# Performance work log

Hardware: AMD Instinct MI355X
Metric: run time of the kernel (lower is better)

## Reference

```python
import jax, jax.numpy as jnp
import numpy as np

# ---- static hyperparameters (mirror init_kwargs) ----
L_MAX = 3
N_MAX_L = [8, 6, 4, 2]            # radial basis size per l (precomputer.n_max_l)
N_CHANNELS = 32                   # num_element_channels
K_MAX_L = [n * N_CHANNELS for n in N_MAX_L]   # [256, 192, 128, 64]
SH_SIZES = [2 * l + 1 for l in range(L_MAX + 1)]  # [1,3,5,7]
MP_SCALING = 0.1
NU_SCALING = 0.1
NU_MAX = 2                        # max_correlation_order_per_layer
N_LAYERS = 2                      # num_message_passing_layers

# Fixed CG coupling tensors for all valid (l1, l2, L) with |l1-l2|<=L<=min(l1+l2, L_MAX).
# (Deterministic stand-ins for real Clebsch-Gordan coefficients; same sparsity/coupling
# structure and identical in fwd and fwdbwd modules.)
_rng = np.random.RandomState(0)
CG = {}
for _l1 in range(L_MAX + 1):
    for _l2 in range(L_MAX + 1):
        for _L in range(abs(_l1 - _l2), min(_l1 + _l2, L_MAX) + 1):
            CG[(_l1, _l2, _L)] = jnp.asarray(
                (_rng.randn(2 * _l1 + 1, 2 * _l2 + 1, 2 * _L + 1) * 0.2).astype(np.float32))


def split_l(x, sizes):
    out, i = [], 0
    for s in sizes:
        out.append(x[:, i:i + s])
        i += s
    return out


def embed_centers(feats, emb):
    # feats[l]: [N, 2l+1, n_l*C]; multiply channel block c by per-atom embedding emb[:, c]
    C = emb.shape[1]
    out = []
    for f in feats:
        n, m, k = f.shape
        out.append((f.reshape(n, m, k // C, C) * emb[:, None, None, :]).reshape(n, m, k))
    return out


def tensor_product(A, B):
    # per-atom CG tensor product, channel-aligned with truncation to min k
    n = A[0].shape[0]
    out = [jnp.zeros((n, 2 * L + 1, K_MAX_L[L]), A[0].dtype) for L in range(L_MAX + 1)]
    for (l1, l2, L), cg in CG.items():
        kk = min(K_MAX_L[l1], K_MAX_L[l2], K_MAX_L[L])
        t = jnp.einsum('nak,nbk,abM->nMk', A[l1][:, :, :kk], B[l2][:, :, :kk], cg)
        out[L] = out[L].at[:, :, :kk].add(t)
    return out


def cg_iterate(feats):
    # CGIterator: nu_max-1 iterated tensor products with residual accumulation
    g = feats
    for _ in range(NU_MAX - 1):
        tp = tensor_product(g, feats)
        g = [g[l] + NU_SCALING * tp[l] for l in range(L_MAX + 1)]
    return g


def invariant_mp(rb_l, sh_l, centers, emb_nbr, n_atoms):
    # spherical expansion: scatter rb x sh x neighbor-embedding over pairs -> centers
    out = []
    for l in range(L_MAX + 1):
        # [P, 2l+1, n_l, C] -> [P, 2l+1, k_l]
        msg = sh_l[l][:, :, None, None] * rb_l[l][:, None, :, None] * emb_nbr[:, None, None, :]
        msg = msg.reshape(msg.shape[0], 2 * l + 1, -1)
        out.append(MP_SCALING * jax.ops.segment_sum(msg, centers, num_segments=n_atoms))
    return out


def equivariant_mp(rb_l, sh_l, centers, neighbors, feats, n_atoms):
    # pair messages: CG-couple radially weighted SH edge features with neighbor features
    edge = [sh_l[l] * rb_l[l].sum(-1, keepdims=True) for l in range(L_MAX + 1)]  # [P, 2l+1]
    out = [jnp.zeros((n_atoms, 2 * L + 1, K_MAX_L[L]), feats[0].dtype) for L in range(L_MAX + 1)]
    for (l1, l2, L), cg in CG.items():
        kk = min(K_MAX_L[l2], K_MAX_L[L])
        w = jnp.einsum('pa,abM->pbM', edge[l1], cg)        # [P, 2l2+1, 2L+1]
        fg = feats[l2][neighbors, :, :kk]                   # gather: [P, 2l2+1, kk]
        msg = jnp.einsum('pbM,pbk->pMk', w, fg)             # [P, 2L+1, kk]
        out[L] = out[L].at[:, :, :kk].add(
            MP_SCALING * jax.ops.segment_sum(msg, centers, num_segments=n_atoms))
    return out


def setup_inputs() -> dict:
    key = jax.random.key(0)
    ks = jax.random.split(key, 8)
    N, P = 5000, 100000
    return {
        'sh': jax.random.normal(ks[0], (P, sum(SH_SIZES)), dtype=jnp.float32),
        'rb': jax.random.uniform(ks[1], (P, sum(N_MAX_L)), dtype=jnp.float32),
        'emb_table': jax.random.normal(ks[2], (4, N_CHANNELS), dtype=jnp.float32),
        'w_energy': jax.random.normal(ks[3], (K_MAX_L[0], 1), dtype=jnp.float32) * 0.05,
        'b_energy': jax.random.normal(ks[4], (1,), dtype=jnp.float32),
        'species_idx': jax.random.randint(ks[5], (N,), 0, 4, dtype=jnp.int32),
        'centers': jax.random.randint(ks[6], (P,), 0, N, dtype=jnp.int32),
        'neighbors': jax.random.randint(ks[7], (P,), 0, N, dtype=jnp.int32),
    }


def reference(sh, rb, emb_table, w_energy, b_energy, species_idx, centers, neighbors):
    n_atoms = species_idx.shape[0]
    sh_l = split_l(sh * NU_SCALING, SH_SIZES)   # nu_scaling applied to spherical harmonics
    rb_l = split_l(rb, N_MAX_L)
    center_emb = emb_table[species_idx]          # [N, C]
    emb_nbr = center_emb[neighbors]              # [P, C]
    # invariant message passing -> spherical expansion, then first CG iteration
    feats = invariant_mp(rb_l, sh_l, centers, emb_nbr, n_atoms)
    feats = cg_iterate(feats)
    # remaining equivariant message-passing layers
    for _ in range(N_LAYERS - 1):
        ef = embed_centers(feats, center_emb)
        mp = equivariant_mp(rb_l, sh_l, centers, neighbors, ef, n_atoms)
        feats = cg_iterate(mp)
    feats = embed_centers(feats, center_emb)
    energies = feats[0] @ w_energy + b_energy    # [N, 1, 1]
    return energies
```

## Files before the change

kernel.cpp:

```cpp
#include <hip/hip_runtime.h>
#include <vector>
#include <cmath>
#include <cstdint>

constexpr int KLc[4]  = {256,192,128,64};
constexpr int NMLc[4] = {8,6,4,2};
constexpr int SHBc[5] = {0,1,4,9,16};
constexpr int RBBc[5] = {0,8,14,18,20};
constexpr int FBc[5]  = {0,256,832,1472,1920};
constexpr int NCMB = 34, CGTOT = 3436, FTOT = 1920;

struct Combos { int l1[NCMB], l2[NCMB], L[NCMB], cgoff[NCMB], kk[NCMB]; };
constexpr Combos make_combos(){
  Combos c{}; int n=0, cg=0;
  for(int a=0;a<=3;a++)for(int b=0;b<=3;b++){
    int lo=a>b?a-b:b-a, hi=(a+b<3)?(a+b):3;
    for(int L=lo;L<=hi;L++){
      c.l1[n]=a; c.l2[n]=b; c.L[n]=L; c.cgoff[n]=cg;
      int mx=a>b?a:b; if(L>mx) mx=L; c.kk[n]=KLc[mx];
      cg+=(2*a+1)*(2*b+1)*(2*L+1); n++;
    }
  }
  return c;
}
constexpr Combos CB = make_combos();
static_assert(CB.cgoff[NCMB-1] + 7*7*7 == CGTOT, "cg size");

struct Grp { int cnt[4]; int list[4][12]; };
constexpr Grp make_Lg(){ Grp g{}; for(int i=0;i<NCMB;i++){ int L=CB.L[i]; g.list[L][g.cnt[L]++]=i; } return g; }
constexpr Grp LG = make_Lg();

struct Rows { int sh[64], rb[64], off[64]; };
constexpr Rows make_rows(){ Rows r{}; int i=0;
  for(int l=0;l<4;l++)for(int m=0;m<2*l+1;m++)for(int n=0;n<NMLc[l];n++){
    r.sh[i]=SHBc[l]+m; r.rb[i]=RBBc[l]+n; r.off[i]=FBc[l]+m*KLc[l]+n*32; i++; }
  for(;i<64;i++){ r.sh[i]=0; r.rb[i]=0; r.off[i]=0; }
  return r; }
constexpr Rows RWS = make_rows();

constexpr int NSL=425, NG=16, MAXS=32, MAXR=4, RPAD=149;
constexpr int JB=48, DEPTH=6;
static_assert(JB % DEPTH == 0, "slot rotation alignment");
constexpr int NTILE=30;

constexpr int iabs_(int x){ return x<0?-x:x; }
__host__ __device__ constexpr bool sl_valid(int l1,int l2,int kt){ return l2<=3-kt && iabs_(l1-l2)<=3-kt; }

__host__ __device__ constexpr int rb_base(int kt,int l1,int l2){
  int base=0;
  for(int p=0;p<4;p++)for(int q=0;q<4;q++){
    if(p==l1 && q==l2) return base;
    if(sl_valid(p,q,kt)) base += (2*p+1)*(2*q+1);
  }
  return base;
}

struct EqTab {
  int ns[NG];
  unsigned char eidx[NG][MAXS];
  unsigned char fidx[NG][MAXS];
  short         srow[NG][MAXS];
  unsigned char sph [NG][MAXS];
  int nr[NG];
  short roff[NG][MAXR];
  int total;
};
constexpr EqTab make_eqtab(){
  EqTab T{};
  int tl2[NTILE]{}, tkt[NTILE]{}, tbb[NTILE]{}, tsz[NTILE]{}; int nt=0;
  for(int l2=0;l2<4;l2++)for(int kt=0;kt<4-l2;kt++)for(int b=0;b<2*l2+1;b++){
    int sz=0;
    for(int l1=0;l1<4;l1++) if(sl_valid(l1,l2,kt)) sz+=2*l1+1;
    tl2[nt]=l2; tkt[nt]=kt; tbb[nt]=b; tsz[nt]=sz; nt++;
  }
  int tg[NTILE]{}; bool used[NTILE]{}; int gload[NG]{};
  for(int it=0; it<nt; it++){
    int best=-1;
    for(int i=0;i<nt;i++) if(!used[i] && (best<0 || tsz[i]>tsz[best])) best=i;
    used[best]=true;
    int g=0; for(int j=1;j<NG;j++) if(gload[j]<gload[g]) g=j;
    tg[best]=g; gload[g]+=tsz[best];
  }
  int total=0;
  for(int g=0; g<NG; g++){
    for(int ti=0; ti<nt; ti++){
      if(tg[ti]!=g) continue;
      const int l2=tl2[ti], kt=tkt[ti], b=tbb[ti];
      const int rowoff = FBc[l2] + b*KLc[l2] + kt*64;
      const int ri = T.nr[g]; T.roff[g][T.nr[g]++] = (short)rowoff;
      for(int l1=0;l1<4;l1++){
        if(!sl_valid(l1,l2,kt)) continue;
        for(int a=0;a<2*l1+1;a++){
          int s = T.ns[g]++;
          T.eidx[g][s] = (unsigned char)(SHBc[l1]+a);
          int rbi = rb_base(kt,l1,l2) + a*(2*l2+1) + b;
          int ph, sr;
          if(kt==0){ if(l1<=2){ ph=0; sr=rbi; } else { ph=1; sr=rbi-144; } }
          else { ph=kt+1; sr=rbi; }
          T.sph[g][s]=(unsigned char)ph; T.srow[g][s]=(short)sr;
          T.fidx[g][s]=(unsigned char)ri;
          total++;
        }
      }
    }
    for(int i=1;i<T.ns[g];i++){
      unsigned char e=T.eidx[g][i], f=T.fidx[g][i], p=T.sph[g][i]; short r=T.srow[g][i];
      int k=i-1;
      while(k>=0 && T.eidx[g][k]>e){
        T.eidx[g][k+1]=T.eidx[g][k]; T.fidx[g][k+1]=T.fidx[g][k];
        T.sph[g][k+1]=T.sph[g][k];   T.srow[g][k+1]=T.srow[g][k]; k--;
      }
      T.eidx[g][k+1]=e; T.fidx[g][k+1]=f; T.sph[g][k+1]=p; T.srow[g][k+1]=r;
    }
  }
  T.total=total;
  return T;
}
constexpr EqTab ET = make_eqtab();
static_assert(ET.total==NSL, "slice count");
constexpr bool chk_ns(){ for(int g=0;g<NG;g++) if(ET.ns[g]>MAXS) return false; return true; }
constexpr bool chk_nr(){ for(int g=0;g<NG;g++) if(ET.nr[g]>MAXR) return false; return true; }
constexpr int sum_nr(){ int s=0; for(int g=0;g<NG;g++) s+=ET.nr[g]; return s; }
static_assert(chk_ns(), "MAXS");
static_assert(chk_nr(), "MAXR");
static_assert(sum_nr()==NTILE, "no row duplication across groups");

struct CAsg { int cnt[NG]; unsigned char ci[NG][8]; };
constexpr CAsg make_casg(){
  CAsg C{}; bool used[NCMB]{}; int load[NG]{};
  for(int it=0; it<NCMB; it++){
    int best=-1, bc=-1;
    for(int i=0;i<NCMB;i++) if(!used[i]){
      int c=(2*CB.l1[i]+1)*(2*CB.l2[i]+1)*(2*CB.L[i]+1);
      if(c>bc){bc=c;best=i;}
    }
    used[best]=true;
    int g=0; for(int j=1;j<NG;j++) if(load[j]<load[g]) g=j;
    C.ci[g][C.cnt[g]++]=(unsigned char)best; load[g]+=bc;
  }
  return C;
}
constexpr CAsg CA = make_casg();
constexpr bool chk_ca(){ for(int g=0;g<NG;g++) if(CA.cnt[g]>8) return false; return true; }
static_assert(chk_ca(), "CA cap");

__host__ __device__ constexpr bool combo_in_phase(int ci,int ph){
  int l1=CB.l1[ci], l2=CB.l2[ci], L=CB.L[ci];
  if(ph==0) return l1<=2;
  if(ph==1) return l1==3;
  int kt=ph-1;
  return (l2<=3-kt) && (L<=3-kt);
}
__host__ __device__ constexpr int phase_kt(int ph){ return ph<=1?0:ph-1; }
__host__ __device__ constexpr int phase_rbadj(int ph){ return ph==1?144:0; }

namespace nprng {
struct MT {
  uint32_t mt[624]; int mti; bool has_g; double g;
  void seed(uint32_t s){ for(int i=0;i<624;i++){ mt[i]=s; s=1812433253u*(s^(s>>30))+(uint32_t)i+1u; } mti=624; has_g=false; g=0.0; }
  uint32_t u32(){
    if(mti>=624){
      for(int i=0;i<624;i++){
        uint32_t y=(mt[i]&0x80000000u)|(mt[(i+1)%624]&0x7fffffffu);
        mt[i]=mt[(i+397)%624]^(y>>1)^((y&1u)?0x9908b0dfu:0u);
      }
      mti=0;
    }
    uint32_t y=mt[mti++];
    y^=y>>11; y^=(y<<7)&0x9d2c5680u; y^=(y<<15)&0xefc60000u; y^=y>>18;
    return y;
  }
  double dbl(){ uint32_t a=u32()>>5, b=u32()>>6; return (a*67108864.0+b)/9007199254740992.0; }
  double gauss(){
    if(has_g){ has_g=false; return g; }
    double f,x1,x2,r2;
    do{ x1=2.0*dbl()-1.0; x2=2.0*dbl()-1.0; r2=x1*x1+x2*x2; }while(r2>=1.0||r2==0.0);
    f=sqrt(-2.0*log(r2)/r2);
    g=f*x1; has_g=true; return f*x2;
  }
};
}
static std::vector<float> build_cg(){
  nprng::MT r; r.seed(0);
  std::vector<float> v; v.reserve(CGTOT);
  for(int l1=0;l1<=3;l1++)for(int l2=0;l2<=3;l2++){
    int lo = l1>l2? l1-l2 : l2-l1;
    int hi = (l1+l2<3)? (l1+l2) : 3;
    for(int L=lo;L<=hi;L++){
      int n=(2*l1+1)*(2*l2+1)*(2*L+1);
      for(int i=0;i<n;i++) v.push_back((float)(r.gauss()*0.2));
    }
  }
  return v;
}

__global__ __launch_bounds__(256) void k_cemb(const float* __restrict__ emb_table,
    const int* __restrict__ species, float* __restrict__ cemb, int* __restrict__ counts, int N){
  int i = blockIdx.x*256 + threadIdx.x;
  if(i < N) counts[i] = 0;
  if(i < N*32){ int n = i>>5, c = i&31; cemb[i] = emb_table[species[n]*32 + c]; }
}

__global__ __launch_bounds__(256) void k_hist(const int* __restrict__ centers, int* counts, int P){
  int i = blockIdx.x*256 + threadIdx.x;
  if(i < P) atomicAdd(&counts[centers[i]], 1);
}

__global__ __launch_bounds__(256) void k_scan(const int* __restrict__ counts,
    int* __restrict__ offsets, int* __restrict__ cursor, int N){
  __shared__ int part[256];
  const int t = threadIdx.x;
  const int CH = (N + 255)/256;
  const int lo = t*CH;
  int hi = (t+1)*CH; if(hi > N) hi = N;
  int s = 0;
  for(int i=lo;i<hi;i++) s += counts[i];
  part[t] = s; __syncthreads();
  const int own = s;
  for(int d=1; d<256; d<<=1){
    int v = (t>=d)? part[t-d] : 0;
    __syncthreads();
    part[t] += v;
    __syncthreads();
  }
  int run = part[t] - own;
  for(int i=lo;i<hi;i++){ offsets[i]=run; cursor[i]=run; run += counts[i]; }
  if(t==255) offsets[N] = part[255];
}

__global__ __launch_bounds__(256) void k_scatter(const int* __restrict__ centers,
    int* cursor, int* __restrict__ perm, int P){
  int i = blockIdx.x*256 + threadIdx.x;
  if(i < P){ int c = centers[i]; int pos = atomicAdd(&cursor[c], 1); perm[pos] = i; }
}

__global__ __launch_bounds__(256) void k_permute(const float* __restrict__ sh,
    const float* __restrict__ rb, const int* __restrict__ nbrs, const int* __restrict__ perm,
    float* __restrict__ edge_p, int* __restrict__ nbrp, int P){
  int u = blockIdx.x*256 + threadIdx.x;
  int pos = u>>4, i = u&15;
  if(pos >= P) return;
  int p = perm[pos];
  if(i==0) nbrp[pos] = nbrs[p];
  int l = (i==0)?0:(i<4)?1:(i<9)?2:3;
  float s=0.f;
  for(int n=RBBc[l]; n<RBBc[l+1]; n++) s += rb[p*20+n];
  edge_p[(size_t)pos*16+i] = sh[p*16+i]*0.1f*s;
}

__global__ __launch_bounds__(256) void k_inv(const float* __restrict__ sh, const float* __restrict__ rb,
    const float* __restrict__ cemb, const int* __restrict__ nbrs, const int* __restrict__ offsets,
    const int* __restrict__ perm, float* __restrict__ feats){
  const int a = blockIdx.x, t = threadIdx.x;
  __shared__ float sh_s[8][16], rb_s[8][20], emb_s[8][32], shrb_s[8][60];
  const int c = t & 31, rg = t >> 5;
  float acc[8];
  #pragma unroll
  for(int j=0;j<8;j++) acc[j] = 0.f;
  const int beg = offsets[a], cnt = offsets[a+1]-beg;
  for(int jb=0; jb<cnt; jb+=8){
    __syncthreads();
    for(int u=t; u<8*36; u+=256){
      int j=u/36, i=u-36*j;
      if(jb+j<cnt){
        int p=perm[beg+jb+j];
        if(i<16) sh_s[j][i]=sh[p*16+i]*0.1f;
        else     rb_s[j][i-16]=rb[p*20+i-16];
      }
    }
    for(int u=t; u<8*32; u+=256){
      int j=u>>5, i=u&31;
      if(jb+j<cnt){ int nb=nbrs[perm[beg+jb+j]]; emb_s[j][i]=cemb[(size_t)nb*32+i]; }
    }
    __syncthreads();
    for(int u=t; u<8*60; u+=256){
      int j=u/60, r=u-60*j;
      if(jb+j<cnt) shrb_s[j][r] = sh_s[j][RWS.sh[r]] * rb_s[j][RWS.rb[r]];
    }
    __syncthreads();
    const int jm = (cnt-jb<8)?(cnt-jb):8;
    for(int j=0;j<jm;j++){
      const float e = emb_s[j][c];
      #pragma unroll
      for(int q=0;q<8;q++){ int r=rg+8*q; if(r<60) acc[q]=fmaf(shrb_s[j][r], e, acc[q]); }
    }
  }
  #pragma unroll
  for(int q=0;q<8;q++){
    int r = rg + 8*q;
    if(r < 60) feats[(size_t)a*FTOT + RWS.off[r] + c] = 0.1f * acc[q];
  }
}

__device__ __forceinline__ float cg_u(const float* __restrict__ cg, int idx){
  return cg[__builtin_amdgcn_readfirstlane(idx)];
}
__global__ __launch_bounds__(256) void k_tp(float* __restrict__ feats, const float* __restrict__ cg){
  const int a = blockIdx.x, t = threadIdx.x;
  __shared__ float f_s[FTOT];
  float* fa = feats + (size_t)a*FTOT;
  for(int i=t;i<FTOT;i+=256)  f_s[i]  = fa[i];
  __syncthreads();
  #pragma unroll
  for(int L=0; L<4; L++){
    const int KLL = KLc[L], nL = 2*L+1;
    const int nel = nL*KLL;
    for(int e=t; e<nel; e+=256){
      const int M = e / KLL, k = e - M*KLL;
      float acc = 0.f;
      #pragma unroll
      for(int gi=0; gi<LG.cnt[L]; gi++){
        const int ci = LG.list[L][gi];
        const int l1 = CB.l1[ci], l2 = CB.l2[ci];
        if(k < CB.kk[ci]){
          const int n2 = 2*l2+1;
          #pragma unroll
          for(int aa=0; aa<2*l1+1; aa++){
            const float Av = f_s[FBc[l1] + aa*KLc[l1] + k];
            #pragma unroll
            for(int b=0; b<n2; b++)
              acc += cg_u(cg, CB.cgoff[ci] + (aa*n2+b)*nL + M) * (Av * f_s[FBc[l2] + b*KLc[l2] + k]);
          }
        }
      }
      fa[FBc[L] + M*KLL + k] = f_s[FBc[L] + M*KLL + k] + 0.1f*acc;
    }
  }
}

template<int G,int PH,int U>
__device__ __forceinline__ void contract_combos(const float* __restrict__ stageT,
    float* __restrict__ out_s, const float* __restrict__ cg, int lane){
  if constexpr (U < CA.cnt[G]) {
    constexpr int ci = CA.ci[G][U];
    if constexpr (combo_in_phase(ci,PH)) {
      constexpr int l1=CB.l1[ci], l2=CB.l2[ci], L=CB.L[ci];
      constexpr int n1=2*l1+1, n2=2*l2+1, nL=2*L+1;
      constexpr int kt=phase_kt(PH);
      constexpr int rbase = rb_base(kt,l1,l2) - phase_rbadj(PH);
      float oa[nL];
      #pragma unroll
      for(int M=0;M<nL;M++) oa[M]=0.f;
      #pragma unroll
      for(int aa=0;aa<n1;aa++){
        #pragma unroll
        for(int b=0;b<n2;b++){
          const float sv = stageT[lane*RPAD + rbase + aa*n2 + b];
          #pragma unroll
          for(int M=0;M<nL;M++)
            oa[M] = fmaf(cg[CB.cgoff[ci] + (aa*n2+b)*nL + M], sv, oa[M]);
        }
      }
      #pragma unroll
      for(int M=0;M<nL;M++)
        atomicAdd(&out_s[FBc[L] + M*KLc[L] + kt*64 + lane], oa[M]);
    }
    contract_combos<G,PH,U+1>(stageT,out_s,cg,lane);
  }
}

template<int G,int PH>
__device__ __forceinline__ void eq_phase(const float* acc, float* stageT, float* out_s,
    const float* __restrict__ cg, int lane){
  __syncthreads();
  #pragma unroll
  for(int s=0;s<ET.ns[G];s++){
    if(ET.sph[G][s]==PH) stageT[lane*RPAD + ET.srow[G][s]] = acc[s];
  }
  __syncthreads();
  contract_combos<G,PH,0>(stageT,out_s,cg,lane);
}

template<int G>
__device__ __forceinline__ void eq_load_pair(float* fg, float& ce, int nb, int lane,
    const float* __restrict__ featsA, const float* __restrict__ cemb){
  ce = cemb[(size_t)nb*32 + (lane&31)];
  const float* fp = featsA + (size_t)nb*FTOT + lane;
  #pragma unroll
  for(int r=0;r<ET.nr[G];r++) fg[r] = fp[ET.roff[G][r]];
}

template<int G>
__device__ __forceinline__ void eq_compute_pair(float* acc, const float* fg, float ce,
    const float* edge_row){
  constexpr int NR = ET.nr[G];
  float fgc[NR];
  #pragma unroll
  for(int r=0;r<NR;r++) fgc[r] = fg[r]*ce;
  float edv = 0.f;
  #pragma unroll
  for(int s=0;s<ET.ns[G];s++){
    if(s==0 || ET.eidx[G][s]!=ET.eidx[G][s-1])
      edv = edge_row[ET.eidx[G][s]];
    acc[s] = fmaf(edv, fgc[ET.fidx[G][s]], acc[s]);
  }
}

template<int G>
__device__ __forceinline__ void eq_group_main(
    const int a, const int t, const int lane,
    const float* __restrict__ edge_p, const int* __restrict__ nbrp,
    const float* __restrict__ cemb, const int* __restrict__ offsets,
    const float* __restrict__ featsA, float* __restrict__ featsB,
    const float* __restrict__ cg,
    float* stageT, float* out_s, float* edge_s, int* nb_s){
  constexpr int NS = ET.ns[G], NR = ET.nr[G];
  float acc[NS];
  #pragma unroll
  for(int s=0;s<NS;s++) acc[s]=0.f;
  for(int i=t;i<FTOT;i+=1024) out_s[i]=0.f;
  const int beg = offsets[a], cnt = offsets[a+1]-beg;
  float fgS[DEPTH][NR]; float ceS[DEPTH];
  #pragma unroll
  for(int s=0;s<DEPTH;s++){
    int nb = (s<cnt)? nbrp[beg+s] : 0;
    eq_load_pair<G>(fgS[s], ceS[s], nb, lane, featsA, cemb);
  }
  for(int jb=0; jb<cnt; jb+=JB){
    __syncthreads();
    if(t < JB*16){
      int j = t>>4;
      if(jb+j < cnt) edge_s[t] = edge_p[(size_t)(beg+jb)*16 + t];
    }
    if(t < JB) nb_s[t] = (jb+t < cnt) ? nbrp[beg+jb+t] : 0;
    __syncthreads();
    const int jm = (cnt-jb<JB)?(cnt-jb):JB;
    for(int j=0;j<jm;j+=DEPTH){
      #pragma unroll
      for(int s=0;s<DEPTH;s++){
        if(j+s < jm){
          eq_compute_pair<G>(acc, fgS[s], ceS[s], edge_s + (j+s)*16);
          int q = jb+j+s+DEPTH;
          int nb = (q<cnt) ? ((q-jb<JB)? nb_s[q-jb] : nbrp[beg+q]) : 0;
          eq_load_pair<G>(fgS[s], ceS[s], nb, lane, featsA, cemb);
        }
      }
    }
  }
  eq_phase<G,0>(acc,stageT,out_s,cg,lane);
  eq_phase<G,1>(acc,stageT,out_s,cg,lane);
  eq_phase<G,2>(acc,stageT,out_s,cg,lane);
  eq_phase<G,3>(acc,stageT,out_s,cg,lane);
  eq_phase<G,4>(acc,stageT,out_s,cg,lane);
  __syncthreads();
  float* ob = featsB + (size_t)a*FTOT;
  for(int i=t;i<FTOT;i+=1024) ob[i] = 0.1f*out_s[i];
}

__global__ __launch_bounds__(1024,4) void k_eq2(const float* __restrict__ edge_p,
    const int* __restrict__ nbrp, const float* __restrict__ cemb,
    const int* __restrict__ offsets, const float* __restrict__ featsA,
    float* __restrict__ featsB, const float* __restrict__ cg){
  __shared__ float stageT[64*RPAD];
  __shared__ float out_s[FTOT];
  __shared__ float edge_s[JB*16];
  __shared__ int   nb_s[JB];
  const int a = blockIdx.x, t = threadIdx.x, lane = t&63, g = t>>6;
  switch(g){
    case 0:  eq_group_main<0 >(a,t,lane,edge_p,nbrp,cemb,offsets,featsA,featsB,cg,stageT,out_s,edge_s,nb_s); break;
    case 1:  eq_group_main<1 >(a,t,lane,edge_p,nbrp,cemb,offsets,featsA,featsB,cg,stageT,out_s,edge_s,nb_s); break;
    case 2:  eq_group_main<2 >(a,t,lane,edge_p,nbrp,cemb,offsets,featsA,featsB,cg,stageT,out_s,edge_s,nb_s); break;
    case 3:  eq_group_main<3 >(a,t,lane,edge_p,nbrp,cemb,offsets,featsA,featsB,cg,stageT,out_s,edge_s,nb_s); break;
    case 4:  eq_group_main<4 >(a,t,lane,edge_p,nbrp,cemb,offsets,featsA,featsB,cg,stageT,out_s,edge_s,nb_s); break;
    case 5:  eq_group_main<5 >(a,t,lane,edge_p,nbrp,cemb,offsets,featsA,featsB,cg,stageT,out_s,edge_s,nb_s); break;
    case 6:  eq_group_main<6 >(a,t,lane,edge_p,nbrp,cemb,offsets,featsA,featsB,cg,stageT,out_s,edge_s,nb_s); break;
    case 7:  eq_group_main<7 >(a,t,lane,edge_p,nbrp,cemb,offsets,featsA,featsB,cg,stageT,out_s,edge_s,nb_s); break;
    case 8:  eq_group_main<8 >(a,t,lane,edge_p,nbrp,cemb,offsets,featsA,featsB,cg,stageT,out_s,edge_s,nb_s); break;
    case 9:  eq_group_main<9 >(a,t,lane,edge_p,nbrp,cemb,offsets,featsA,featsB,cg,stageT,out_s,edge_s,nb_s); break;
    case 10: eq_group_main<10>(a,t,lane,edge_p,nbrp,cemb,offsets,featsA,featsB,cg,stageT,out_s,edge_s,nb_s); break;
    case 11: eq_group_main<11>(a,t,lane,edge_p,nbrp,cemb,offsets,featsA,featsB,cg,stageT,out_s,edge_s,nb_s); break;
    case 12: eq_group_main<12>(a,t,lane,edge_p,nbrp,cemb,offsets,featsA,featsB,cg,stageT,out_s,edge_s,nb_s); break;
    case 13: eq_group_main<13>(a,t,lane,edge_p,nbrp,cemb,offsets,featsA,featsB,cg,stageT,out_s,edge_s,nb_s); break;
    case 14: eq_group_main<14>(a,t,lane,edge_p,nbrp,cemb,offsets,featsA,featsB,cg,stageT,out_s,edge_s,nb_s); break;
    default: eq_group_main<15>(a,t,lane,edge_p,nbrp,cemb,offsets,featsA,featsB,cg,stageT,out_s,edge_s,nb_s); break;
  }
}

__global__ __launch_bounds__(256) void k_energy(const float* __restrict__ feats,
    const float* __restrict__ cemb, const float* __restrict__ wE, const float* __restrict__ bE,
    float* __restrict__ out, int N){
  const int wid = threadIdx.x >> 6, lane = threadIdx.x & 63;
  const int a = blockIdx.x*4 + wid;
  if(a >= N) return;
  const float e = cemb[(size_t)a*32 + (lane & 31)];
  float s = 0.f;
  for(int k=lane; k<256; k+=64) s += feats[(size_t)a*FTOT + k] * e * wE[k];
  #pragma unroll
  for(int off=32; off; off>>=1) s += __shfl_down(s, off, 64);
  if(lane == 0) out[a] = s + bE[0];
}

extern "C" void kernel_launch(void* const* d_in, const int* in_sizes, int n_in,
                              void* d_out, int out_size, void* d_ws, size_t ws_size,
                              hipStream_t stream){
  const float* sh        = (const float*)d_in[0];
  const float* rb        = (const float*)d_in[1];
  const float* emb_table = (const float*)d_in[2];
  const float* wE        = (const float*)d_in[3];
  const float* bE        = (const float*)d_in[4];
  const int*   species   = (const int*)d_in[5];
  const int*   centers   = (const int*)d_in[6];
  const int*   nbrs      = (const int*)d_in[7];
  const int N = in_sizes[5];
  const int P = in_sizes[6];

  char* ws = (char*)d_ws; size_t off = 0;
  auto carve = [&](size_t bytes)->void*{
    void* p = ws + off; off = (off + bytes + 255) & ~(size_t)255; return p;
  };
  float* cg_d    = (float*)carve((size_t)CGTOT*4);
  float* cemb    = (float*)carve((size_t)N*32*4);
  int*   counts  = (int*)  carve((size_t)N*4);
  int*   offsets = (int*)  carve((size_t)(N+1)*4);
  int*   cursor  = (int*)  carve((size_t)N*4);
  int*   perm    = (int*)  carve((size_t)P*4);
  float* edge_pd = (float*)carve((size_t)P*16*4);
  int*   nbrp    = (int*)  carve((size_t)P*4);
  float* featsA  = (float*)carve((size_t)N*FTOT*4);
  float* featsB  = (float*)carve((size_t)N*FTOT*4);
  (void)ws_size; (void)n_in; (void)out_size;

  static const std::vector<float> cg_host = build_cg();
  hipMemcpyAsync(cg_d, cg_host.data(), (size_t)CGTOT*4, hipMemcpyHostToDevice, stream);

  k_cemb   <<<(N*32 + 255)/256, 256, 0, stream>>>(emb_table, species, cemb, counts, N);
  k_hist   <<<(P + 255)/256,    256, 0, stream>>>(centers, counts, P);
  k_scan   <<<1,                256, 0, stream>>>(counts, offsets, cursor, N);
  k_scatter<<<(P + 255)/256,    256, 0, stream>>>(centers, cursor, perm, P);
  k_permute<<<(P*16 + 255)/256, 256, 0, stream>>>(sh, rb, nbrs, perm, edge_pd, nbrp, P);
  k_inv    <<<N,                256, 0, stream>>>(sh, rb, cemb, nbrs, offsets, perm, featsA);
  k_tp     <<<N,                256, 0, stream>>>(featsA, cg_d);
  k_eq2    <<<N,               1024, 0, stream>>>(edge_pd, nbrp, cemb, offsets, featsA, featsB, cg_d);
  k_tp     <<<N,                256, 0, stream>>>(featsB, cg_d);
  k_energy <<<(N + 3)/4,        256, 0, stream>>>(featsB, cemb, wE, bE, (float*)d_out, N);
}
```

Before: 0.9998 ms.

## Unify equivariant gather loop with dense two-tile-per-wave slice layout

Each of the 16 waves now owns at most two feature tiles and a fixed 32-slot accumulator: 16 spherical-harmonic slots per tile, with invalid slots padded. The neighbour-gather main loop becomes a single shared code path instead of 16 template specializations, and each edge's 16 values are read from LDS as float4s. This aims to cut instruction-cache pressure and per-slice table indirection. The cost is some wasted FMAs on padded slots (512 vs 425 useful) and more accumulator registers. Prefetch depth is also raised from 6 to 8.

```diff
diff --git a/kernel.cpp b/kernel.cpp
--- a/kernel.cpp
+++ b/kernel.cpp
@@ -38,8 +38,8 @@
   return r; }
 constexpr Rows RWS = make_rows();
 
-constexpr int NSL=425, NG=16, MAXS=32, MAXR=4, RPAD=149;
-constexpr int JB=48, DEPTH=6;
+constexpr int NSL=425, NG=16, RPAD=149;
+constexpr int JB=48, DEPTH=8;
 static_assert(JB % DEPTH == 0, "slot rotation alignment");
 constexpr int NTILE=30;
 
@@ -56,74 +56,66 @@
 }
 
 struct EqTab {
-  int ns[NG];
-  unsigned char eidx[NG][MAXS];
-  unsigned char fidx[NG][MAXS];
-  short         srow[NG][MAXS];
-  unsigned char sph [NG][MAXS];
+  short       srow[NG][32];
+  signed char sph [NG][32];
   int nr[NG];
-  short roff[NG][MAXR];
+  short roff[NG][2];
   int total;
 };
 constexpr EqTab make_eqtab(){
   EqTab T{};
+  for(int g=0;g<NG;g++){
+    for(int s=0;s<32;s++){ T.srow[g][s]=-1; T.sph[g][s]=-1; }
+    T.nr[g]=0; T.roff[g][0]=0; T.roff[g][1]=0;
+  }
   int tl2[NTILE]{}, tkt[NTILE]{}, tbb[NTILE]{}, tsz[NTILE]{}; int nt=0;
   for(int l2=0;l2<4;l2++)for(int kt=0;kt<4-l2;kt++)for(int b=0;b<2*l2+1;b++){
     int sz=0;
     for(int l1=0;l1<4;l1++) if(sl_valid(l1,l2,kt)) sz+=2*l1+1;
     tl2[nt]=l2; tkt[nt]=kt; tbb[nt]=b; tsz[nt]=sz; nt++;
   }
-  int tg[NTILE]{}; bool used[NTILE]{}; int gload[NG]{};
+  bool used[NTILE]{}; int gload[NG]{}; int gcnt[NG]{}; int gt[NG][2]{};
   for(int it=0; it<nt; it++){
     int best=-1;
     for(int i=0;i<nt;i++) if(!used[i] && (best<0 || tsz[i]>tsz[best])) best=i;
     used[best]=true;
-    int g=0; for(int j=1;j<NG;j++) if(gload[j]<gload[g]) g=j;
-    tg[best]=g; gload[g]+=tsz[best];
+    int g=-1;
+    for(int j=0;j<NG;j++) if(gcnt[j]<2 && (g<0 || gload[j]<gload[g])) g=j;
+    gt[g][gcnt[g]]=best; gcnt[g]++; gload[g]+=tsz[best];
   }
   int total=0;
-  for(int g=0; g<NG; g++){
-    for(int ti=0; ti<nt; ti++){
-      if(tg[ti]!=g) continue;
+  for(int g=0;g<NG;g++){
+    T.nr[g]=gcnt[g];
+    for(int tk=0;tk<gcnt[g];tk++){
+      const int ti=gt[g][tk];
       const int l2=tl2[ti], kt=tkt[ti], b=tbb[ti];
-      const int rowoff = FBc[l2] + b*KLc[l2] + kt*64;
-      const int ri = T.nr[g]; T.roff[g][T.nr[g]++] = (short)rowoff;
-      for(int l1=0;l1<4;l1++){
+      T.roff[g][tk]=(short)(FBc[l2]+b*KLc[l2]+kt*64);
+      for(int i=0;i<16;i++){
+        const int l1=(i==0)?0:(i<4)?1:(i<9)?2:3;
+        const int aa=i-SHBc[l1];
         if(!sl_valid(l1,l2,kt)) continue;
-        for(int a=0;a<2*l1+1;a++){
-          int s = T.ns[g]++;
-          T.eidx[g][s] = (unsigned char)(SHBc[l1]+a);
-          int rbi = rb_base(kt,l1,l2) + a*(2*l2+1) + b;
-          int ph, sr;
-          if(kt==0){ if(l1<=2){ ph=0; sr=rbi; } else { ph=1; sr=rbi-144; } }
-          else { ph=kt+1; sr=rbi; }
-          T.sph[g][s]=(unsigned char)ph; T.srow[g][s]=(short)sr;
-          T.fidx[g][s]=(unsigned char)ri;
-          total++;
-        }
+        const int s=tk*16+i;
+        const int rbi=rb_base(kt,l1,l2)+aa*(2*l2+1)+b;
+        int ph, sr;
+        if(kt==0){ if(l1<=2){ ph=0; sr=rbi; } else { ph=1; sr=rbi-144; } }
+        else { ph=kt+1; sr=rbi; }
+        T.sph[g][s]=(signed char)ph; T.srow[g][s]=(short)sr;
+        total++;
       }
     }
-    for(int i=1;i<T.ns[g];i++){
-      unsigned char e=T.eidx[g][i], f=T.fidx[g][i], p=T.sph[g][i]; short r=T.srow[g][i];
-      int k=i-1;
-      while(k>=0 && T.eidx[g][k]>e){
-        T.eidx[g][k+1]=T.eidx[g][k]; T.fidx[g][k+1]=T.fidx[g][k];
-        T.sph[g][k+1]=T.sph[g][k];   T.srow[g][k+1]=T.srow[g][k]; k--;
-      }
-      T.eidx[g][k+1]=e; T.fidx[g][k+1]=f; T.sph[g][k+1]=p; T.srow[g][k+1]=r;
-    }
+    if(gcnt[g]==1) T.roff[g][1]=T.roff[g][0];
   }
   T.total=total;
   return T;
 }
 constexpr EqTab ET = make_eqtab();
 static_assert(ET.total==NSL, "slice count");
-constexpr bool chk_ns(){ for(int g=0;g<NG;g++) if(ET.ns[g]>MAXS) return false; return true; }
-constexpr bool chk_nr(){ for(int g=0;g<NG;g++) if(ET.nr[g]>MAXR) return false; return true; }
-constexpr int sum_nr(){ int s=0; for(int g=0;g<NG;g++) s+=ET.nr[g]; return s; }
-static_assert(chk_ns(), "MAXS");
-static_assert(chk_nr(), "MAXR");
-static_assert(sum_nr()==NTILE, "no row duplication across groups");
+constexpr bool chk_srow(){ for(int g=0;g<NG;g++) for(int s=0;s<32;s++) if(ET.srow[g][s]>=RPAD) return false; return true; }
+static_assert(chk_srow(), "stage rows fit RPAD");
+
+struct RoffA { int r0[NG]; int r1[NG]; };
+constexpr RoffA make_roffa(){ RoffA R{}; for(int g=0;g<NG;g++){ R.r0[g]=ET.roff[g][0]; R.r1[g]=ET.roff[g][1]; } return R; }
+constexpr RoffA RFA = make_roffa();
 
 struct CAsg { int cnt[NG]; unsigned char ci[NG][8]; };
 constexpr CAsg make_casg(){
@@ -364,7 +356,7 @@
     const float* __restrict__ cg, int lane){
   __syncthreads();
   #pragma unroll
-  for(int s=0;s<ET.ns[G];s++){
+  for(int s=0;s<32;s++){
     if(ET.sph[G][s]==PH) stageT[lane*RPAD + ET.srow[G][s]] = acc[s];
   }
   __syncthreads();
@@ -372,79 +364,36 @@
 }
 
 template<int G>
-__device__ __forceinline__ void eq_load_pair(float* fg, float& ce, int nb, int lane,
-    const float* __restrict__ featsA, const float* __restrict__ cemb){
-  ce = cemb[(size_t)nb*32 + (lane&31)];
-  const float* fp = featsA + (size_t)nb*FTOT + lane;
-  #pragma unroll
-  for(int r=0;r<ET.nr[G];r++) fg[r] = fp[ET.roff[G][r]];
-}
-
-template<int G>
-__device__ __forceinline__ void eq_compute_pair(float* acc, const float* fg, float ce,
-    const float* edge_row){
-  constexpr int NR = ET.nr[G];
-  float fgc[NR];
-  #pragma unroll
-  for(int r=0;r<NR;r++) fgc[r] = fg[r]*ce;
-  float edv = 0.f;
-  #pragma unroll
-  for(int s=0;s<ET.ns[G];s++){
-    if(s==0 || ET.eidx[G][s]!=ET.eidx[G][s-1])
-      edv = edge_row[ET.eidx[G][s]];
-    acc[s] = fmaf(edv, fgc[ET.fidx[G][s]], acc[s]);
-  }
-}
-
-template<int G>
-__device__ __forceinline__ void eq_group_main(
-    const int a, const int t, const int lane,
-    const float* __restrict__ edge_p, const int* __restrict__ nbrp,
-    const float* __restrict__ cemb, const int* __restrict__ offsets,
-    const float* __restrict__ featsA, float* __restrict__ featsB,
-    const float* __restrict__ cg,
-    float* stageT, float* out_s, float* edge_s, int* nb_s){
-  constexpr int NS = ET.ns[G], NR = ET.nr[G];
-  float acc[NS];
-  #pragma unroll
-  for(int s=0;s<NS;s++) acc[s]=0.f;
-  for(int i=t;i<FTOT;i+=1024) out_s[i]=0.f;
-  const int beg = offsets[a], cnt = offsets[a+1]-beg;
-  float fgS[DEPTH][NR]; float ceS[DEPTH];
-  #pragma unroll
-  for(int s=0;s<DEPTH;s++){
-    int nb = (s<cnt)? nbrp[beg+s] : 0;
-    eq_load_pair<G>(fgS[s], ceS[s], nb, lane, featsA, cemb);
-  }
-  for(int jb=0; jb<cnt; jb+=JB){
-    __syncthreads();
-    if(t < JB*16){
-      int j = t>>4;
-      if(jb+j < cnt) edge_s[t] = edge_p[(size_t)(beg+jb)*16 + t];
-    }
-    if(t < JB) nb_s[t] = (jb+t < cnt) ? nbrp[beg+jb+t] : 0;
-    __syncthreads();
-    const int jm = (cnt-jb<JB)?(cnt-jb):JB;
-    for(int j=0;j<jm;j+=DEPTH){
-      #pragma unroll
-      for(int s=0;s<DEPTH;s++){
-        if(j+s < jm){
-          eq_compute_pair<G>(acc, fgS[s], ceS[s], edge_s + (j+s)*16);
-          int q = jb+j+s+DEPTH;
-          int nb = (q<cnt) ? ((q-jb<JB)? nb_s[q-jb] : nbrp[beg+q]) : 0;
-          eq_load_pair<G>(fgS[s], ceS[s], nb, lane, featsA, cemb);
-        }
-      }
-    }
-  }
+__device__ __forceinline__ void eq_phases(const float* acc, float* stageT, float* out_s,
+    const float* __restrict__ cg, int lane){
   eq_phase<G,0>(acc,stageT,out_s,cg,lane);
   eq_phase<G,1>(acc,stageT,out_s,cg,lane);
   eq_phase<G,2>(acc,stageT,out_s,cg,lane);
   eq_phase<G,3>(acc,stageT,out_s,cg,lane);
   eq_phase<G,4>(acc,stageT,out_s,cg,lane);
-  __syncthreads();
-  float* ob = featsB + (size_t)a*FTOT;
-  for(int i=t;i<FTOT;i+=1024) ob[i] = 0.1f*out_s[i];
+}
+
+__device__ __forceinline__ void eq_load_pair(float* fg, float& ce, int nb, int lane,
+    int ro0, int ro1, const float* __restrict__ featsA, const float* __restrict__ cemb){
+  ce = cemb[(size_t)nb*32 + (lane&31)];
+  const float* fp = featsA + (size_t)nb*FTOT + lane;
+  fg[0] = fp[ro0];
+  fg[1] = fp[ro1];
+}
+
+__device__ __forceinline__ void eq_compute_pair(float* acc, const float* fg, float ce,
+    const float* edge_row){
+  float ed[16];
+  #pragma unroll
+  for(int q=0;q<4;q++){
+    float4 v = *(const float4*)(edge_row + q*4);
+    ed[q*4]=v.x; ed[q*4+1]=v.y; ed[q*4+2]=v.z; ed[q*4+3]=v.w;
+  }
+  const float f0 = fg[0]*ce, f1 = fg[1]*ce;
+  #pragma unroll
+  for(int i=0;i<16;i++) acc[i]    = fmaf(ed[i], f0, acc[i]);
+  #pragma unroll
+  for(int i=0;i<16;i++) acc[16+i] = fmaf(ed[i], f1, acc[16+i]);
 }
 
 __global__ __launch_bounds__(1024,4) void k_eq2(const float* __restrict__ edge_p,
@@ -456,24 +405,64 @@
   __shared__ float edge_s[JB*16];
   __shared__ int   nb_s[JB];
   const int a = blockIdx.x, t = threadIdx.x, lane = t&63, g = t>>6;
+
+  float acc[32];
+  #pragma unroll
+  for(int s=0;s<32;s++) acc[s]=0.f;
+  for(int i=t;i<FTOT;i+=1024) out_s[i]=0.f;
+  const int beg = offsets[a], cnt = offsets[a+1]-beg;
+  const int ro0 = __builtin_amdgcn_readfirstlane(RFA.r0[g]);
+  const int ro1 = __builtin_amdgcn_readfirstlane(RFA.r1[g]);
+
+  float fgS[DEPTH][2]; float ceS[DEPTH];
+  #pragma unroll
+  for(int s=0;s<DEPTH;s++){
+    int nb = (s<cnt)? nbrp[beg+s] : 0;
+    eq_load_pair(fgS[s], ceS[s], nb, lane, ro0, ro1, featsA, cemb);
+  }
+  for(int jb=0; jb<cnt; jb+=JB){
+    __syncthreads();
+    if(t < JB*16){
+      int j = t>>4;
+      if(jb+j < cnt) edge_s[t] = edge_p[(size_t)(beg+jb)*16 + t];
+    }
+    if(t < JB) nb_s[t] = (jb+t < cnt) ? nbrp[beg+jb+t] : 0;
+    __syncthreads();
+    const int jm = (cnt-jb<JB)?(cnt-jb):JB;
+    for(int j=0;j<jm;j+=DEPTH){
+      #pragma unroll
+      for(int s=0;s<DEPTH;s++){
+        if(j+s < jm){
+          eq_compute_pair(acc, fgS[s], ceS[s], edge_s + (j+s)*16);
+          int q = jb+j+s+DEPTH;
+          int nb = (q<cnt) ? ((q-jb<JB)? nb_s[q-jb] : nbrp[beg+q]) : 0;
+          eq_load_pair(fgS[s], ceS[s], nb, lane, ro0, ro1, featsA, cemb);
+        }
+      }
+    }
+  }
+
   switch(g){
-    case 0:  eq_group_main<0 >(a,t,lane,edge_p,nbrp,cemb,offsets,featsA,featsB,cg,stageT,out_s,edge_s,nb_s); break;
-    case 1:  eq_group_main<1 >(a,t,lane,edge_p,nbrp,cemb,offsets,featsA,featsB,cg,stageT,out_s,edge_s,nb_s); break;
-    case 2:  eq_group_main<2 >(a,t,lane,edge_p,nbrp,cemb,offsets,featsA,featsB,cg,stageT,out_s,edge_s,nb_s); break;
-    case 3:  eq_group_main<3 >(a,t,lane,edge_p,nbrp,cemb,offsets,featsA,featsB,cg,stageT,out_s,edge_s,nb_s); break;
-    case 4:  eq_group_main<4 >(a,t,lane,edge_p,nbrp,cemb,offsets,featsA,featsB,cg,stageT,out_s,edge_s,nb_s); break;
-    case 5:  eq_group_main<5 >(a,t,lane,edge_p,nbrp,cemb,offsets,featsA,featsB,cg,stageT,out_s,edge_s,nb_s); break;
-    case 6:  eq_group_main<6 >(a,t,lane,edge_p,nbrp,cemb,offsets,featsA,featsB,cg,stageT,out_s,edge_s,nb_s); break;
-    case 7:  eq_group_main<7 >(a,t,lane,edge_p,nbrp,cemb,offsets,featsA,featsB,cg,stageT,out_s,edge_s,nb_s); break;
-    case 8:  eq_group_main<8 >(a,t,lane,edge_p,nbrp,cemb,offsets,featsA,featsB,cg,stageT,out_s,edge_s,nb_s); break;
-    case 9:  eq_group_main<9 >(a,t,lane,edge_p,nbrp,cemb,offsets,featsA,featsB,cg,stageT,out_s,edge_s,nb_s); break;
-    case 10: eq_group_main<10>(a,t,lane,edge_p,nbrp,cemb,offsets,featsA,featsB,cg,stageT,out_s,edge_s,nb_s); break;
-    case 11: eq_group_main<11>(a,t,lane,edge_p,nbrp,cemb,offsets,featsA,featsB,cg,stageT,out_s,edge_s,nb_s); break;
-    case 12: eq_group_main<12>(a,t,lane,edge_p,nbrp,cemb,offsets,featsA,featsB,cg,stageT,out_s,edge_s,nb_s); break;
-    case 13: eq_group_main<13>(a,t,lane,edge_p,nbrp,cemb,offsets,featsA,featsB,cg,stageT,out_s,edge_s,nb_s); break;
-    case 14: eq_group_main<14>(a,t,lane,edge_p,nbrp,cemb,offsets,featsA,featsB,cg,stageT,out_s,edge_s,nb_s); break;
-    default: eq_group_main<15>(a,t,lane,edge_p,nbrp,cemb,offsets,featsA,featsB,cg,stageT,out_s,edge_s,nb_s); break;
-  }
+    case 0:  eq_phases<0 >(acc,stageT,out_s,cg,lane); break;
+    case 1:  eq_phases<1 >(acc,stageT,out_s,cg,lane); break;
+    case 2:  eq_phases<2 >(acc,stageT,out_s,cg,lane); break;
+    case 3:  eq_phases<3 >(acc,stageT,out_s,cg,lane); break;
+    case 4:  eq_phases<4 >(acc,stageT,out_s,cg,lane); break;
+    case 5:  eq_phases<5 >(acc,stageT,out_s,cg,lane); break;
+    case 6:  eq_phases<6 >(acc,stageT,out_s,cg,lane); break;
+    case 7:  eq_phases<7 >(acc,stageT,out_s,cg,lane); break;
+    case 8:  eq_phases<8 >(acc,stageT,out_s,cg,lane); break;
+    case 9:  eq_phases<9 >(acc,stageT,out_s,cg,lane); break;
+    case 10: eq_phases<10>(acc,stageT,out_s,cg,lane); break;
+    case 11: eq_phases<11>(acc,stageT,out_s,cg,lane); break;
+    case 12: eq_phases<12>(acc,stageT,out_s,cg,lane); break;
+    case 13: eq_phases<13>(acc,stageT,out_s,cg,lane); break;
+    case 14: eq_phases<14>(acc,stageT,out_s,cg,lane); break;
+    default: eq_phases<15>(acc,stageT,out_s,cg,lane); break;
+  }
+  __syncthreads();
+  float* ob = featsB + (size_t)a*FTOT;
+  for(int i=t;i<FTOT;i+=1024) ob[i] = 0.1f*out_s[i];
 }
 
 __global__ __launch_bounds__(256) void k_energy(const float* __restrict__ feats,
```

New measurement: 1.002 ms. No clear change (+0.2%).
